# Optimization experiments

Measured on AMD Instinct MI355X. Metric: run time of the kernel, lower is better.

Reference implementation:

```python
import jax, jax.numpy as jnp
import numpy as np

N_E = 8192
E_DIM = 256
BETA = 0.25


def setup_inputs() -> dict:
    key = jax.random.key(0)
    k_z, k_w = jax.random.split(key)
    z = jax.random.normal(k_z, (32, E_DIM, 32, 32), dtype=jnp.float32)
    # nn.Embedding weight init: uniform(-1/n_e, 1/n_e)
    W = jax.random.uniform(k_w, (N_E, E_DIM), dtype=jnp.float32,
                           minval=-1.0 / N_E, maxval=1.0 / N_E)
    return {"z": z, "W": W}


def reference(z, W):
    B, C, H, Wd = z.shape
    beta = jnp.float32(BETA)
    z_nhwc = jnp.transpose(z, (0, 2, 3, 1))          # (B,H,W,C)
    zf = z_nhwc.reshape(-1, C)                       # (N,C)
    # squared-distance matrix (N, n_e)
    d = (jnp.sum(zf * zf, axis=1, keepdims=True)
         + jnp.sum(W * W, axis=1)
         - 2.0 * jnp.matmul(zf, W.T))
    idx = jnp.argmin(d, axis=1)                      # (N,)
    # one-hot @ W == gather
    z_q = W[idx].reshape(z_nhwc.shape)               # (B,H,W,C)
    loss = (jnp.mean((jax.lax.stop_gradient(z_q) - z_nhwc) ** 2)
            + beta * jnp.mean((z_q - jax.lax.stop_gradient(z_nhwc)) ** 2))
    # straight-through estimator
    z_q = z_nhwc + jax.lax.stop_gradient(z_q - z_nhwc)
    # codebook usage perplexity
    n = idx.shape[0]
    e_mean = jnp.zeros((N_E,), jnp.float32).at[idx].add(1.0) / n
    perplexity = jnp.exp(-jnp.sum(e_mean * jnp.log(e_mean + 1e-10)))
    z_q = jnp.transpose(z_q, (0, 3, 1, 2))           # back to (B,C,H,W)
    index = idx.reshape(B, H, Wd)
    return z_q, loss, index, perplexity
```

## Files before the change

kernel.cpp:

```cpp
#include <hip/hip_runtime.h>
#include <float.h>
#include <math.h>

#define OUT_LOSS 8388608
#define OUT_IDX  8388609
#define OUT_PERP 8421377

#define WS_ZH    0ull
#define WS_ZL    16777216ull
#define WS_ZT    0ull
#define WS_WH    33554432ull
#define WS_S     37748736ull
#define WS_B     37879808ull
#define WS_MAXW  37912576ull
#define WS_IDX   37912640ull
#define WS_HIST  38043712ull
#define WS_CAND  38076480ull
#define WS_FULL  38469696ull
#define WS_FKEY  38600768ull
#define WS_CNT   38862912ull
#define WS_LOSS  38862920ull

typedef short v8s __attribute__((ext_vector_type(8)));
typedef float v4f __attribute__((ext_vector_type(4)));

__device__ __forceinline__ unsigned short bf16rne(float f) {
  unsigned u = __float_as_uint(f);
  return (unsigned short)((u + 0x7FFFu + ((u >> 16) & 1u)) >> 16);
}
__device__ __forceinline__ float bf16tof(unsigned short h) {
  return __uint_as_float(((unsigned)h) << 16);
}

__device__ __forceinline__ void gl_lds16(const void* g, void* l) {
  __builtin_amdgcn_global_load_lds(
      (const __attribute__((address_space(1))) unsigned int*)g,
      (__attribute__((address_space(3))) unsigned int*)l, 16, 0, 0);
}

__global__ void k_zero(int* __restrict__ hist, unsigned long long* __restrict__ fkey,
                       int* __restrict__ cnt, double* __restrict__ loss,
                       unsigned* __restrict__ maxw) {
  const int i = blockIdx.x * 256 + threadIdx.x;
  if (i < 8192) hist[i] = 0;
  else if (i < 40960) fkey[i - 8192] = ~0ull;
  else if (i == 40960) cnt[0] = 0;
  else if (i == 40961) cnt[1] = 0;
  else if (i == 40962) *loss = 0.0;
  else if (i == 40963) *maxw = 0u;
}

__global__ __launch_bounds__(256) void k_split(const float* __restrict__ W,
                                               unsigned short* __restrict__ Wh) {
  const int u = blockIdx.x * 256 + threadIdx.x;
  const int kc = u >> 15, grp = (u >> 6) & 511, q = (u >> 4) & 3, col = u & 15;
  const int j = grp * 16 + col, k0 = kc * 32 + q * 8;
  const float4 w0 = *(const float4*)(W + (size_t)j * 256 + k0);
  const float4 w1 = *(const float4*)(W + (size_t)j * 256 + k0 + 4);
  const float wv[8] = {w0.x, w0.y, w0.z, w0.w, w1.x, w1.y, w1.z, w1.w};
  unsigned short h[8] __attribute__((aligned(16)));
#pragma unroll
  for (int i = 0; i < 8; ++i) h[i] = bf16rne(wv[i]);
  *(uint4*)(Wh + (size_t)u * 8) = *(const uint4*)h;
}

__global__ __launch_bounds__(256) void k_splitz(const float* __restrict__ z,
    unsigned short* __restrict__ Zh, unsigned short* __restrict__ Zl) {
  const int gt = blockIdx.x * 256 + threadIdx.x;
  const int kc = gt >> 15;
  const int n  = gt & 32767;
  const int b = n >> 10, p = n & 1023;
  const float* zp = z + (size_t)b * 262144 + (size_t)(kc * 32) * 1024 + p;
  unsigned short hh[32] __attribute__((aligned(16)));
  unsigned short ll[32] __attribute__((aligned(16)));
#pragma unroll
  for (int i = 0; i < 32; ++i) {
    const float v = zp[(size_t)i * 1024];
    const unsigned short h = bf16rne(v);
    hh[i] = h;
    ll[i] = bf16rne(__fsub_rn(v, bf16tof(h)));
  }
  const size_t o = (size_t)kc * 1048576 + (size_t)(n >> 4) * 512 + (size_t)(n & 15) * 8;
#pragma unroll
  for (int q = 0; q < 4; ++q) *(uint4*)(Zh + o + q * 128) = *(const uint4*)(hh + q * 8);
#pragma unroll
  for (int q = 0; q < 4; ++q) *(uint4*)(Zl + o + q * 128) = *(const uint4*)(ll + q * 8);
}

__global__ __launch_bounds__(256) void k_zt(const float* __restrict__ z,
                                            float* __restrict__ zT) {
  const int gt = blockIdx.x * 256 + threadIdx.x;
  const int kc = gt >> 15;
  const int n  = gt & 32767;
  const int b = n >> 10, p = n & 1023;
  const float* zp = z + (size_t)b * 262144 + (size_t)(kc * 32) * 1024 + p;
  float v[32] __attribute__((aligned(16)));
#pragma unroll
  for (int i = 0; i < 32; ++i) v[i] = zp[(size_t)i * 1024];
  float* dst = zT + (size_t)n * 256 + kc * 32;
#pragma unroll
  for (int j = 0; j < 8; ++j) *(float4*)(dst + j * 4) = *(const float4*)(v + j * 4);
}

__device__ __forceinline__ float np_sumsq256(const float* __restrict__ base,
                                             const int stride) {
  float h[2];
#pragma unroll
  for (int half = 0; half < 2; ++half) {
    const float* a = base + (size_t)(half * 128) * stride;
    float r[8];
#pragma unroll
    for (int k = 0; k < 8; ++k) { const float v = a[(size_t)k * stride]; r[k] = __fmul_rn(v, v); }
    for (int i = 8; i < 128; i += 8) {
#pragma unroll
      for (int k = 0; k < 8; ++k) {
        const float v = a[(size_t)(i + k) * stride];
        r[k] = __fadd_rn(r[k], __fmul_rn(v, v));
      }
    }
    h[half] = __fadd_rn(
        __fadd_rn(__fadd_rn(r[0], r[1]), __fadd_rn(r[2], r[3])),
        __fadd_rn(__fadd_rn(r[4], r[5]), __fadd_rn(r[6], r[7])));
  }
  return __fadd_rn(h[0], h[1]);
}

__global__ __launch_bounds__(256) void k_sz(const float* __restrict__ z,
                                            float* __restrict__ S) {
  const int n = blockIdx.x * 256 + threadIdx.x;
  S[n] = np_sumsq256(z + (size_t)(n >> 10) * 262144 + (n & 1023), 1024);
}

__global__ __launch_bounds__(256) void k_wsq(const float* __restrict__ W,
                                             float* __restrict__ B,
                                             unsigned* __restrict__ maxw) {
  const int j = blockIdx.x * 256 + threadIdx.x;
  const float b = np_sumsq256(W + (size_t)j * 256, 1);
  B[j] = b;
  atomicMax(maxw, __float_as_uint(b));
}

__device__ __forceinline__ void merge5(float& a1, int& ai1, float& a2, int& ai2,
                                       float& a3, float b1, int bi1, float b2,
                                       int bi2, float b3) {
  const bool t1 = (b1 < a1) || (b1 == a1 && bi1 < ai1);
  const float w2v = t1 ? b2 : a2; const int w2i = t1 ? bi2 : ai2;
  const float w3v = t1 ? b3 : a3;
  const float l1v = t1 ? a1 : b1; const int l1i = t1 ? ai1 : bi1;
  const float l2v = t1 ? a2 : b2;
  const float n1v = t1 ? b1 : a1; const int n1i = t1 ? bi1 : ai1;
  const bool t2 = (w2v < l1v) || (w2v == l1v && w2i < l1i);
  a1 = n1v; ai1 = n1i;
  a2 = t2 ? w2v : l1v; ai2 = t2 ? w2i : l1i;
  a3 = t2 ? fminf(w3v, l1v) : fminf(w2v, l2v);
}

#define AH_OFF 0
#define AL_OFF 32768
#define B0_OFF 65536
#define B1_OFF 98304
#define SC_OFF 65536
__global__ __launch_bounds__(512, 2) void k_main(
    const unsigned short* __restrict__ Zh, const unsigned short* __restrict__ Zl,
    const unsigned short* __restrict__ Wh, const float* __restrict__ S,
    const float* __restrict__ B, const unsigned* __restrict__ maxw,
    int* __restrict__ idxb, int* __restrict__ cand, int* __restrict__ full,
    int* __restrict__ cnt) {
  extern __shared__ __align__(16) char smem[];
  const int t = threadIdx.x;
  const int w = t >> 6, lane = t & 63, col = lane & 15, q = lane >> 4;
  const int phalf = w >> 2, strip = w & 3;
  const int n0 = blockIdx.x << 6;

  {
    const size_t ab = (size_t)w * 1048576 + (size_t)(n0 >> 4) * 512 + (size_t)lane * 8;
    char* dh = smem + AH_OFF + w * 4096;
    char* dl = smem + AL_OFF + w * 4096;
#pragma unroll
    for (int i = 0; i < 4; ++i) gl_lds16(Zh + ab + (size_t)i * 512, dh + i * 1024);
#pragma unroll
    for (int i = 0; i < 4; ++i) gl_lds16(Zl + ab + (size_t)i * 512, dl + i * 1024);
  }
  {
    const size_t bb = (size_t)(w * 4) * 512 + (size_t)lane * 8;
#pragma unroll
    for (int i = 0; i < 4; ++i)
      gl_lds16(Wh + bb + (size_t)i * 512, smem + B0_OFF + (w * 4 + i) * 1024);
  }
  __syncthreads();

  float spx[8];
#pragma unroll
  for (int s = 0; s < 8; ++s)
    spx[s] = S[n0 + phalf * 32 + (s >> 2) * 16 + q * 4 + (s & 3)];

  float m1[8], m2[8], m3[8]; int i1[8], i2[8];
#pragma unroll
  for (int s = 0; s < 8; ++s) {
    m1[s] = FLT_MAX; m2[s] = FLT_MAX; m3[s] = FLT_MAX;
    i1[s] = 0x7fffffff; i2[s] = 0x7fffffff;
  }

  v4f acc[2][8];
#pragma unroll
  for (int pt = 0; pt < 2; ++pt)
#pragma unroll
    for (int nt = 0; nt < 8; ++nt) acc[pt][nt] = (v4f){0.f, 0.f, 0.f, 0.f};

  for (int it = 0; it < 128; ++it) {
    const int ct = it >> 3, kc = it & 7;
    if (it < 127) {
      const int nct = (it + 1) >> 3, nkc = (it + 1) & 7;
      const size_t cb = (size_t)nkc * 262144 + (size_t)nct * 16384
                      + (size_t)(w * 4) * 512 + (size_t)lane * 8;
      char* nbuf = smem + (((it + 1) & 1) ? B1_OFF : B0_OFF) + (w * 4) * 1024;
#pragma unroll
      for (int i = 0; i < 4; ++i)
        gl_lds16(Wh + cb + (size_t)i * 512, nbuf + i * 1024);
    }
    const char* bbuf = smem + ((it & 1) ? B1_OFF : B0_OFF);
    v8s ah[2], al[2];
#pragma unroll
    for (int pt = 0; pt < 2; ++pt) {
      const int g = phalf * 2 + pt;
      ah[pt] = *(const v8s*)(smem + AH_OFF + kc * 4096 + g * 1024 + lane * 16);
      al[pt] = *(const v8s*)(smem + AL_OFF + kc * 4096 + g * 1024 + lane * 16);
    }
#pragma unroll
    for (int nt = 0; nt < 8; ++nt) {
      const v8s bh = *(const v8s*)(bbuf + (strip * 8 + nt) * 1024 + lane * 16);
#pragma unroll
      for (int pt = 0; pt < 2; ++pt) {
        acc[pt][nt] = __builtin_amdgcn_mfma_f32_16x16x32_bf16(ah[pt], bh, acc[pt][nt], 0, 0, 0);
        acc[pt][nt] = __builtin_amdgcn_mfma_f32_16x16x32_bf16(al[pt], bh, acc[pt][nt], 0, 0, 0);
      }
    }
    __syncthreads();
    if (kc == 7) {
#pragma unroll
      for (int nt = 0; nt < 8; ++nt) {
        const int code = ct * 512 + strip * 128 + nt * 16 + col;
        const float bb = B[code];
#pragma unroll
        for (int pt = 0; pt < 2; ++pt) {
          const v4f a = acc[pt][nt];
#pragma unroll
          for (int r = 0; r < 4; ++r) {
            const int s = pt * 4 + r;
            const float d = __fsub_rn(__fadd_rn(spx[s], bb), __fmul_rn(2.f, a[r]));
            const bool c1 = (d < m1[s]);
            const bool c2 = (d < m2[s]);
            const bool c3 = (d < m3[s]);
            m3[s] = c2 ? m2[s] : (c3 ? d : m3[s]);
            m2[s] = c1 ? m1[s] : (c2 ? d : m2[s]);
            i2[s] = c1 ? i1[s] : (c2 ? code : i2[s]);
            m1[s] = c1 ? d : m1[s];
            i1[s] = c1 ? code : i1[s];
          }
        }
#pragma unroll
        for (int pt = 0; pt < 2; ++pt) acc[pt][nt] = (v4f){0.f, 0.f, 0.f, 0.f};
      }
    }
  }

#pragma unroll
  for (int s = 0; s < 8; ++s) {
    for (int msk = 1; msk < 16; msk <<= 1) {
      const float b1 = __shfl_xor(m1[s], msk, 16);
      const int  bi1 = __shfl_xor(i1[s], msk, 16);
      const float b2 = __shfl_xor(m2[s], msk, 16);
      const int  bi2 = __shfl_xor(i2[s], msk, 16);
      const float b3 = __shfl_xor(m3[s], msk, 16);
      merge5(m1[s], i1[s], m2[s], i2[s], m3[s], b1, bi1, b2, bi2, b3);
    }
  }
  __syncthreads();
  float* sc = (float*)(smem + SC_OFF);
  if (col == 0) {
#pragma unroll
    for (int s = 0; s < 8; ++s) {
      const int px = phalf * 32 + (s >> 2) * 16 + q * 4 + (s & 3);
      const int base = (px * 4 + strip) * 5;
      sc[base]     = m1[s];
      sc[base + 1] = __int_as_float(i1[s]);
      sc[base + 2] = m2[s];
      sc[base + 3] = __int_as_float(i2[s]);
      sc[base + 4] = m3[s];
    }
  }
  __syncthreads();
  if (t < 64) {
    const int base0 = t * 20;
    float A1 = sc[base0], A2 = sc[base0 + 2], A3 = sc[base0 + 4];
    int AI1 = __float_as_int(sc[base0 + 1]), AI2 = __float_as_int(sc[base0 + 3]);
    for (int st = 1; st < 4; ++st) {
      const int base = base0 + st * 5;
      merge5(A1, AI1, A2, AI2, A3, sc[base], __float_as_int(sc[base + 1]),
             sc[base + 2], __float_as_int(sc[base + 3]), sc[base + 4]);
    }
    const int n = n0 + t;
    idxb[n] = AI1;
    const float nw = sqrtf(S[n]) * sqrtf(__uint_as_float(*maxw));
    const float win = 2.0f * (0.001953125f * nw + 1e-6f)
                    + 2.0f * ldexpf(1.0f, ilogbf(fmaxf(A1, 1e-30f)) - 23);
    if (A2 <= A1 + win) {
      if (A3 <= A1 + win) {
        const int p = atomicAdd(&cnt[1], 1);
        full[p] = n;
      } else {
        const int p = atomicAdd(&cnt[0], 1);
        cand[3 * p] = n; cand[3 * p + 1] = AI1; cand[3 * p + 2] = AI2;
      }
    }
  }
}

__global__ __launch_bounds__(256) void k_cand(const float* __restrict__ zT,
    const float* __restrict__ W, const float* __restrict__ S,
    const float* __restrict__ B, const int* __restrict__ cand,
    const int* __restrict__ cnt, int* __restrict__ idxb) {
  const int e = blockIdx.x * 256 + threadIdx.x;
  if (e >= cnt[0]) return;
  const int n = cand[3 * e], ca = cand[3 * e + 1], cb = cand[3 * e + 2];
  const float* zp = zT + (size_t)n * 256;
  const float* wa = W + (size_t)ca * 256;
  const float* wb = W + (size_t)cb * 256;
  float a1 = 0.f, a2 = 0.f;
  for (int c = 0; c < 256; ++c) {
    const float zv = zp[c];
    a1 = __builtin_fmaf(zv, wa[c], a1);
    a2 = __builtin_fmaf(zv, wb[c], a2);
  }
  const float d1 = __fsub_rn(__fadd_rn(S[n], B[ca]), __fmul_rn(2.f, a1));
  const float d2 = __fsub_rn(__fadd_rn(S[n], B[cb]), __fmul_rn(2.f, a2));
  idxb[n] = (d1 < d2) ? ca : ((d2 < d1) ? cb : min(ca, cb));
}

__global__ __launch_bounds__(256) void k_full(const float* __restrict__ zT,
    const float* __restrict__ W, const float* __restrict__ S,
    const float* __restrict__ B, const int* __restrict__ full,
    const int* __restrict__ cnt, unsigned long long* __restrict__ fkey) {
  extern __shared__ __align__(16) char fsm[];
  float* zsf = (float*)fsm;
  float* wt  = (float*)(fsm + 32768);
  float* mv  = (float*)(fsm + 32768 + 32896);
  int*   mi  = (int*)(fsm + 32768 + 32896 + 4224);
  const int t = threadIdx.x;
  const int pg = t & 7, cg = t >> 3;
  const int fN = min(cnt[1], 32768);
  const int units = ((fN + 31) >> 5) << 5;
  for (int e = blockIdx.x; e < units; e += 2048) {
    const int g = e >> 5, tt = e & 31;
    const int c0 = tt << 8;
    __syncthreads();
    {
      const int px = t >> 3, c8 = t & 7;
      const int f = (g << 5) + px;
      const int n = (f < fN) ? full[f] : full[0];
      const float4* src = (const float4*)(zT + (size_t)n * 256 + c8 * 32);
      const int colq = (((px >> 2) ^ c8) << 2) + (px & 3);
#pragma unroll
      for (int j = 0; j < 8; ++j) {
        const float4 v = src[j];
        const int c = c8 * 32 + j * 4;
        zsf[(c    ) * 32 + colq] = v.x;
        zsf[(c + 1) * 32 + colq] = v.y;
        zsf[(c + 2) * 32 + colq] = v.z;
        zsf[(c + 3) * 32 + colq] = v.w;
      }
    }
    float s4[4];
#pragma unroll
    for (int i = 0; i < 4; ++i) {
      const int f = (g << 5) + (pg << 2) + i;
      s4[i] = (f < fN) ? S[full[f]] : 0.f;
    }
    float bm[4]; int bj[4];
#pragma unroll
    for (int i = 0; i < 4; ++i) { bm[i] = FLT_MAX; bj[i] = 0x7fffffff; }
    float acc[4][8];
#pragma unroll
    for (int i = 0; i < 4; ++i)
#pragma unroll
      for (int u = 0; u < 8; ++u) acc[i][u] = 0.f;
    for (int kc = 0; kc < 8; ++kc) {
      const int kb = kc << 5;
      __syncthreads();
#pragma unroll
      for (int p = 0; p < 8; ++p) {
        const int jl = (t >> 3) + (p << 5);
        const float4 wv4 =
            *(const float4*)&W[(size_t)(c0 + jl) * 256 + kb + ((t & 7) << 2)];
        const int k0 = (t & 7) << 2;
        wt[(k0    ) * 257 + jl] = wv4.x;
        wt[(k0 + 1) * 257 + jl] = wv4.y;
        wt[(k0 + 2) * 257 + jl] = wv4.z;
        wt[(k0 + 3) * 257 + jl] = wv4.w;
      }
      __syncthreads();
      const int zq = ((pg ^ kc) & 7) << 2;
      for (int k = 0; k < 32; ++k) {
        const float4 z4 = *(const float4*)&zsf[(kb + k) * 32 + zq];
        const float4 wA = *(const float4*)&wt[k * 257 + (cg << 3)];
        const float4 wB = *(const float4*)&wt[k * 257 + (cg << 3) + 4];
        const float zv[4] = {z4.x, z4.y, z4.z, z4.w};
        const float wv[8] = {wA.x, wA.y, wA.z, wA.w, wB.x, wB.y, wB.z, wB.w};
#pragma unroll
        for (int i = 0; i < 4; ++i)
#pragma unroll
          for (int u = 0; u < 8; ++u)
            acc[i][u] = __builtin_fmaf(zv[i], wv[u], acc[i][u]);
      }
    }
#pragma unroll
    for (int u = 0; u < 8; ++u) {
      const int code = c0 + (cg << 3) + u;
      const float bb = B[code];
#pragma unroll
      for (int i = 0; i < 4; ++i) {
        const float d = __fsub_rn(__fadd_rn(s4[i], bb), __fmul_rn(2.f, acc[i][u]));
        if (d < bm[i]) { bm[i] = d; bj[i] = code; }
      }
    }
    __syncthreads();
#pragma unroll
    for (int i = 0; i < 4; ++i) {
      const int px = (pg << 2) + i;
      mv[px * 33 + cg] = bm[i];
      mi[px * 33 + cg] = bj[i];
    }
    __syncthreads();
    if (t < 32) {
      float m = mv[t * 33]; int j = mi[t * 33];
      for (int c = 1; c < 32; ++c) {
        const float v = mv[t * 33 + c]; const int vi = mi[t * 33 + c];
        if (v < m || (v == m && vi < j)) { m = v; j = vi; }
      }
      const int f = (g << 5) + t;
      if (f < fN) {
        const unsigned long long key =
            (((unsigned long long)__float_as_uint(m)) << 13) | (unsigned)j;
        atomicMin(&fkey[f], key);
      }
    }
  }
}

__global__ __launch_bounds__(256) void k_fullfin(const int* __restrict__ full,
    const int* __restrict__ cnt, const unsigned long long* __restrict__ fkey,
    int* __restrict__ idxb) {
  const int f = blockIdx.x * 256 + threadIdx.x;
  if (f < cnt[1]) idxb[full[f]] = (int)(fkey[f] & 8191ull);
}

__global__ __launch_bounds__(256) void k_zq(const float* __restrict__ z,
    const float* __restrict__ W, const int* __restrict__ idxb,
    float* __restrict__ out, double* __restrict__ loss, int* __restrict__ hist) {
  __shared__ float red[256];
  const int t = threadIdx.x;
  const int tx = t & 63, ty = t >> 6;
  const int n0 = blockIdx.x << 6;
  const int n = n0 + tx;
  const int b = n >> 10;
  const int p = n & 1023;
  const int myidx = idxb[n];
  const float* wrow = W + (size_t)myidx * 256;
  float lsum = 0.f;
#pragma unroll 4
  for (int cc = 0; cc < 64; ++cc) {
    const int c = ty * 64 + cc;
    const float qv = wrow[c];
    const size_t off = (size_t)b * 262144 + (size_t)c * 1024 + p;
    const float zv = z[off];
    const float d = __fsub_rn(qv, zv);
    lsum = __builtin_fmaf(d, d, lsum);
    out[off] = __fadd_rn(zv, d);
  }
  red[t] = lsum;
  __syncthreads();
  for (int o = 128; o > 0; o >>= 1) {
    if (t < o) red[t] += red[t + o];
    __syncthreads();
  }
  if (t == 0) atomicAdd(loss, (double)red[0]);
  if (ty == 0) atomicAdd(&hist[myidx], 1);
  if (ty == 1) out[OUT_IDX + n] = (float)myidx;
}

__global__ void k_final(const int* __restrict__ hist,
                        const double* __restrict__ loss,
                        float* __restrict__ out) {
  __shared__ double sh[256];
  const int t = threadIdx.x;
  double s = 0.0;
  for (int j = t; j < 8192; j += 256) {
    const double e = (double)hist[j] / 32768.0;
    s += e * log(e + 1e-10);
  }
  sh[t] = s;
  __syncthreads();
  for (int off = 128; off > 0; off >>= 1) {
    if (t < off) sh[t] += sh[t + off];
    __syncthreads();
  }
  if (t == 0) {
    out[OUT_PERP] = (float)exp(-sh[0]);
    out[OUT_LOSS] = (float)(1.25 * (*loss) / 8388608.0);
  }
}

extern "C" void kernel_launch(void* const* d_in, const int* in_sizes, int n_in,
                              void* d_out, int out_size, void* d_ws, size_t ws_size,
                              hipStream_t stream) {
  const float* z = (const float*)d_in[0];
  const float* W = (const float*)d_in[1];
  float* out = (float*)d_out;
  char* ws = (char*)d_ws;
  unsigned short* Zh = (unsigned short*)(ws + WS_ZH);
  unsigned short* Zl = (unsigned short*)(ws + WS_ZL);
  unsigned short* Wh = (unsigned short*)(ws + WS_WH);
  float*  zT   = (float*)(ws + WS_ZT);
  float*  S    = (float*)(ws + WS_S);
  float*  B    = (float*)(ws + WS_B);
  unsigned* maxw = (unsigned*)(ws + WS_MAXW);
  int*    idxb = (int*)(ws + WS_IDX);
  int*    hist = (int*)(ws + WS_HIST);
  int*    cand = (int*)(ws + WS_CAND);
  int*    full = (int*)(ws + WS_FULL);
  unsigned long long* fkey = (unsigned long long*)(ws + WS_FKEY);
  int*    cnt  = (int*)(ws + WS_CNT);
  double* loss = (double*)(ws + WS_LOSS);

  hipLaunchKernelGGL(k_zero,    dim3(161),  dim3(256), 0, stream, hist, fkey, cnt, loss, maxw);
  hipLaunchKernelGGL(k_split,   dim3(1024), dim3(256), 0, stream, W, Wh);
  hipLaunchKernelGGL(k_splitz,  dim3(1024), dim3(256), 0, stream, z, Zh, Zl);
  hipLaunchKernelGGL(k_sz,      dim3(128),  dim3(256), 0, stream, z, S);
  hipLaunchKernelGGL(k_wsq,     dim3(32),   dim3(256), 0, stream, W, B, maxw);
  hipLaunchKernelGGL(k_main,    dim3(512),  dim3(512), 131072, stream,
                     Zh, Zl, Wh, S, B, maxw, idxb, cand, full, cnt);
  hipLaunchKernelGGL(k_zt,      dim3(1024), dim3(256), 0, stream, z, zT);
  hipLaunchKernelGGL(k_cand,    dim3(128),  dim3(256), 0, stream, zT, W, S, B, cand, cnt, idxb);
  hipLaunchKernelGGL(k_full,    dim3(2048), dim3(256), 74112, stream, zT, W, S, B, full, cnt, fkey);
  hipLaunchKernelGGL(k_fullfin, dim3(128),  dim3(256), 0, stream, full, cnt, fkey, idxb);
  hipLaunchKernelGGL(k_zq,      dim3(512),  dim3(256), 0, stream, z, W, idxb, out, loss, hist);
  hipLaunchKernelGGL(k_final,   dim3(1),    dim3(256), 0, stream, hist, loss, out);
}
```

Baseline: 833.8 us.

## Triple-buffer codebook tiles, keep z-high fragments in registers, stage norms in LDS

Replaces the double-buffered codebook pipeline in the main distance kernel with a three-buffer ring that prefetches two tiles ahead. It waits with explicit vmcnt counts plus a raw barrier instead of a full __syncthreads. The high-part z fragments are loaded once into registers rather than re-read from LDS each step, and the codebook norm vector is staged into LDS for the argmin epilogue. The aim is to hide global-load latency and cut LDS traffic, at the cost of 64 extra VGPRs per thread under a 512x2 launch bound (spill risk) and a larger 160KB LDS footprint.

```diff
diff --git a/kernel.cpp b/kernel.cpp
--- a/kernel.cpp
+++ b/kernel.cpp
@@ -155,10 +155,11 @@
   a3 = t2 ? fminf(w3v, l1v) : fminf(w2v, l2v);
 }
 
-#define AH_OFF 0
-#define AL_OFF 32768
+#define AL_OFF 0
+#define BQ_OFF 32768
 #define B0_OFF 65536
 #define B1_OFF 98304
+#define B2_OFF 131072
 #define SC_OFF 65536
 __global__ __launch_bounds__(512, 2) void k_main(
     const unsigned short* __restrict__ Zh, const unsigned short* __restrict__ Zl,
@@ -172,27 +173,43 @@
   const int phalf = w >> 2, strip = w & 3;
   const int n0 = blockIdx.x << 6;
 
-  {
-    const size_t ab = (size_t)w * 1048576 + (size_t)(n0 >> 4) * 512 + (size_t)lane * 8;
-    char* dh = smem + AH_OFF + w * 4096;
-    char* dl = smem + AL_OFF + w * 4096;
-#pragma unroll
-    for (int i = 0; i < 4; ++i) gl_lds16(Zh + ab + (size_t)i * 512, dh + i * 1024);
-#pragma unroll
-    for (int i = 0; i < 4; ++i) gl_lds16(Zl + ab + (size_t)i * 512, dl + i * 1024);
-  }
-  {
-    const size_t bb = (size_t)(w * 4) * 512 + (size_t)lane * 8;
-#pragma unroll
-    for (int i = 0; i < 4; ++i)
-      gl_lds16(Wh + bb + (size_t)i * 512, smem + B0_OFF + (w * 4 + i) * 1024);
-  }
-  __syncthreads();
-
   float spx[8];
 #pragma unroll
   for (int s = 0; s < 8; ++s)
     spx[s] = S[n0 + phalf * 32 + (s >> 2) * 16 + q * 4 + (s & 3)];
+
+  v8s ah[8][2];
+  const size_t abase = (size_t)(n0 >> 4) * 512 + (size_t)lane * 8;
+#pragma unroll
+  for (int kc = 0; kc < 8; ++kc)
+#pragma unroll
+    for (int pt = 0; pt < 2; ++pt)
+      ah[kc][pt] = *(const v8s*)(Zh + (size_t)kc * 1048576 + abase
+                                 + (size_t)(phalf * 2 + pt) * 512);
+
+  {
+    const size_t ab = (size_t)w * 1048576 + abase;
+    char* dl = smem + AL_OFF + w * 4096;
+#pragma unroll
+    for (int i = 0; i < 4; ++i) gl_lds16(Zl + ab + (size_t)i * 512, dl + i * 1024);
+  }
+  {
+#pragma unroll
+    for (int i = 0; i < 4; ++i)
+      gl_lds16(B + (size_t)i * 2048 + (size_t)w * 256 + (size_t)lane * 4,
+               smem + BQ_OFF + i * 8192 + w * 1024);
+  }
+#pragma unroll
+  for (int c = 0; c < 2; ++c) {
+    const size_t cb = (size_t)(c & 7) * 262144 + (size_t)(w * 4) * 512
+                    + (size_t)lane * 8;
+    char* d = smem + (c ? B1_OFF : B0_OFF) + (w * 4) * 1024;
+#pragma unroll
+    for (int i = 0; i < 4; ++i) gl_lds16(Wh + cb + (size_t)i * 512, d + i * 1024);
+  }
+  asm volatile("s_waitcnt vmcnt(4)" ::: "memory");
+  __builtin_amdgcn_s_barrier();
+  asm volatile("" ::: "memory");
 
   float m1[8], m2[8], m3[8]; int i1[8], i2[8];
 #pragma unroll
@@ -207,60 +224,69 @@
 #pragma unroll
     for (int nt = 0; nt < 8; ++nt) acc[pt][nt] = (v4f){0.f, 0.f, 0.f, 0.f};
 
-  for (int it = 0; it < 128; ++it) {
-    const int ct = it >> 3, kc = it & 7;
-    if (it < 127) {
-      const int nct = (it + 1) >> 3, nkc = (it + 1) & 7;
-      const size_t cb = (size_t)nkc * 262144 + (size_t)nct * 16384
-                      + (size_t)(w * 4) * 512 + (size_t)lane * 8;
-      char* nbuf = smem + (((it + 1) & 1) ? B1_OFF : B0_OFF) + (w * 4) * 1024;
-#pragma unroll
-      for (int i = 0; i < 4; ++i)
-        gl_lds16(Wh + cb + (size_t)i * 512, nbuf + i * 1024);
-    }
-    const char* bbuf = smem + ((it & 1) ? B1_OFF : B0_OFF);
-    v8s ah[2], al[2];
-#pragma unroll
-    for (int pt = 0; pt < 2; ++pt) {
-      const int g = phalf * 2 + pt;
-      ah[pt] = *(const v8s*)(smem + AH_OFF + kc * 4096 + g * 1024 + lane * 16);
-      al[pt] = *(const v8s*)(smem + AL_OFF + kc * 4096 + g * 1024 + lane * 16);
-    }
-#pragma unroll
-    for (int nt = 0; nt < 8; ++nt) {
-      const v8s bh = *(const v8s*)(bbuf + (strip * 8 + nt) * 1024 + lane * 16);
-#pragma unroll
-      for (int pt = 0; pt < 2; ++pt) {
-        acc[pt][nt] = __builtin_amdgcn_mfma_f32_16x16x32_bf16(ah[pt], bh, acc[pt][nt], 0, 0, 0);
-        acc[pt][nt] = __builtin_amdgcn_mfma_f32_16x16x32_bf16(al[pt], bh, acc[pt][nt], 0, 0, 0);
-      }
-    }
-    __syncthreads();
-    if (kc == 7) {
+  char* cur = smem + B0_OFF;
+  char* nxt = smem + B1_OFF;
+  char* nx2 = smem + B2_OFF;
+  const float* bq = (const float*)(smem + BQ_OFF);
+
+  for (int ct = 0; ct < 16; ++ct) {
+#pragma unroll
+    for (int kc = 0; kc < 8; ++kc) {
+      const int it = ct * 8 + kc;
+      if (it < 126) {
+        const int nc = it + 2;
+        const size_t cb = (size_t)(nc & 7) * 262144 + (size_t)(nc >> 3) * 16384
+                        + (size_t)(w * 4) * 512 + (size_t)lane * 8;
+        char* d = nx2 + (w * 4) * 1024;
+#pragma unroll
+        for (int i = 0; i < 4; ++i)
+          gl_lds16(Wh + cb + (size_t)i * 512, d + i * 1024);
+      }
+      v8s al[2];
+#pragma unroll
+      for (int pt = 0; pt < 2; ++pt)
+        al[pt] = *(const v8s*)(smem + AL_OFF + kc * 4096
+                               + (phalf * 2 + pt) * 1024 + lane * 16);
 #pragma unroll
       for (int nt = 0; nt < 8; ++nt) {
-        const int code = ct * 512 + strip * 128 + nt * 16 + col;
-        const float bb = B[code];
+        const v8s bh = *(const v8s*)(cur + (strip * 8 + nt) * 1024 + lane * 16);
 #pragma unroll
         for (int pt = 0; pt < 2; ++pt) {
-          const v4f a = acc[pt][nt];
-#pragma unroll
-          for (int r = 0; r < 4; ++r) {
-            const int s = pt * 4 + r;
-            const float d = __fsub_rn(__fadd_rn(spx[s], bb), __fmul_rn(2.f, a[r]));
-            const bool c1 = (d < m1[s]);
-            const bool c2 = (d < m2[s]);
-            const bool c3 = (d < m3[s]);
-            m3[s] = c2 ? m2[s] : (c3 ? d : m3[s]);
-            m2[s] = c1 ? m1[s] : (c2 ? d : m2[s]);
-            i2[s] = c1 ? i1[s] : (c2 ? code : i2[s]);
-            m1[s] = c1 ? d : m1[s];
-            i1[s] = c1 ? code : i1[s];
+          acc[pt][nt] = __builtin_amdgcn_mfma_f32_16x16x32_bf16(ah[kc][pt], bh, acc[pt][nt], 0, 0, 0);
+          acc[pt][nt] = __builtin_amdgcn_mfma_f32_16x16x32_bf16(al[pt], bh, acc[pt][nt], 0, 0, 0);
+        }
+      }
+      if (kc == 7) {
+#pragma unroll
+        for (int nt = 0; nt < 8; ++nt) {
+          const int code = ct * 512 + strip * 128 + nt * 16 + col;
+          const float bb = bq[code];
+#pragma unroll
+          for (int pt = 0; pt < 2; ++pt) {
+            const v4f a = acc[pt][nt];
+#pragma unroll
+            for (int r = 0; r < 4; ++r) {
+              const int s = pt * 4 + r;
+              const float d = __fsub_rn(__fadd_rn(spx[s], bb), __fmul_rn(2.f, a[r]));
+              const bool c1 = (d < m1[s]);
+              const bool c2 = (d < m2[s]);
+              const bool c3 = (d < m3[s]);
+              m3[s] = c2 ? m2[s] : (c3 ? d : m3[s]);
+              m2[s] = c1 ? m1[s] : (c2 ? d : m2[s]);
+              i2[s] = c1 ? i1[s] : (c2 ? code : i2[s]);
+              m1[s] = c1 ? d : m1[s];
+              i1[s] = c1 ? code : i1[s];
+            }
           }
+#pragma unroll
+          for (int pt = 0; pt < 2; ++pt) acc[pt][nt] = (v4f){0.f, 0.f, 0.f, 0.f};
         }
-#pragma unroll
-        for (int pt = 0; pt < 2; ++pt) acc[pt][nt] = (v4f){0.f, 0.f, 0.f, 0.f};
-      }
+      }
+      if (it < 126) asm volatile("s_waitcnt vmcnt(4)" ::: "memory");
+      else          asm volatile("s_waitcnt vmcnt(0)" ::: "memory");
+      __builtin_amdgcn_s_barrier();
+      asm volatile("" ::: "memory");
+      char* tmp = cur; cur = nxt; nxt = nx2; nx2 = tmp;
     }
   }
 
@@ -537,7 +563,7 @@
   hipLaunchKernelGGL(k_splitz,  dim3(1024), dim3(256), 0, stream, z, Zh, Zl);
   hipLaunchKernelGGL(k_sz,      dim3(128),  dim3(256), 0, stream, z, S);
   hipLaunchKernelGGL(k_wsq,     dim3(32),   dim3(256), 0, stream, W, B, maxw);
-  hipLaunchKernelGGL(k_main,    dim3(512),  dim3(512), 131072, stream,
+  hipLaunchKernelGGL(k_main,    dim3(512),  dim3(512), 163840, stream,
                      Zh, Zl, Wh, S, B, maxw, idxb, cand, full, cnt);
   hipLaunchKernelGGL(k_zt,      dim3(1024), dim3(256), 0, stream, z, zT);
   hipLaunchKernelGGL(k_cand,    dim3(128),  dim3(256), 0, stream, zT, W, S, B, cand, cnt, idxb);
```

Measured after the change: 822.3 us. No clear change (-1.4%).
